# Performance work log

Measured on AMD Instinct MI355X. Metric: run time of the kernel, lower is better.

The kernel has to match this reference:

```python
import jax, jax.numpy as jnp
import numpy as np

N = 100000   # nodes
E = 640000   # edges
D = 128      # in_channels
C = 40       # out_channels (classes)


def setup_inputs() -> dict:
    key = jax.random.key(0)
    ks = jax.random.split(key, 6)
    x = jax.random.normal(ks[0], (N, D), jnp.float32)
    edge_index = jax.random.randint(ks[1], (2, E), 0, N)
    edge_weight = jax.random.uniform(ks[2], (E,), jnp.float32)
    # 8 block convs (4 blocks x 2) stacked, + final conv
    Wb = jax.random.normal(ks[3], (8, D, D), jnp.float32) / np.sqrt(D)
    bb = jnp.zeros((8, D), jnp.float32)
    Wf = jax.random.normal(ks[4], (D, C), jnp.float32) / np.sqrt(D)
    bf = jnp.zeros((C,), jnp.float32)
    return dict(x=x, edge_index=edge_index, edge_weight=edge_weight,
                Wb=Wb, bb=bb, Wf=Wf, bf=bf)


def _gcn(x, W, b, src, dst, w):
    """PyG GCNConv (normalize=True) with self-loops already appended to src/dst/w."""
    n = x.shape[0]
    h = x @ W                                   # [N, out]
    deg = jax.ops.segment_sum(w, dst, num_segments=n)
    dinv = jnp.where(deg > 0, jax.lax.rsqrt(deg), 0.0)
    norm = dinv[src] * w * dinv[dst]            # [E+N]
    out = jax.ops.segment_sum(h[src] * norm[:, None], dst, num_segments=n)
    return out + b


def reference(x, edge_index, edge_weight, Wb, bb, Wf, bf):
    n = x.shape[0]
    loop = jnp.arange(n)
    src = jnp.concatenate([edge_index[0], loop])
    dst = jnp.concatenate([edge_index[1], loop])
    w = jnp.concatenate([edge_weight, jnp.ones((n,), x.dtype)])
    # forward only runs blocks 1-4 (blocks 5-7 unused in the original forward)
    for i in range(4):
        identity = x
        x = jax.nn.relu(_gcn(x, Wb[2 * i], bb[2 * i], src, dst, w))
        # dropout: identity in eval mode
        x = jax.nn.relu(_gcn(x, Wb[2 * i + 1], bb[2 * i + 1], src, dst, w))
        # F.normalize: row-wise L2 with eps=1e-12
        x = x / jnp.maximum(jnp.linalg.norm(x, axis=1, keepdims=True), 1e-12)
        x = (x + identity) / 2
    x = _gcn(x, Wf, bf, src, dst, w)
    return jax.nn.log_softmax(x, axis=1)
```

## Files before the change

### kernel.cpp

```cpp
#include <hip/hip_runtime.h>
#include <math.h>

#define NN 100000
#define EE 640000
#define DD 128
#define CC 40
#define FIXS 4194304.0f

typedef __bf16 bf16x8 __attribute__((ext_vector_type(8)));
typedef float f32x4 __attribute__((ext_vector_type(4)));
typedef unsigned short us8 __attribute__((ext_vector_type(8)));

__device__ inline unsigned short f2b(float f) {
    union { float f; unsigned u; } v; v.f = f;
    unsigned u = v.u;
    return (unsigned short)((u + 0x7FFFu + ((u >> 16) & 1u)) >> 16);
}
__device__ inline float b2f(unsigned short b) {
    union { unsigned u; float f; } v; v.u = ((unsigned)b) << 16;
    return v.f;
}


__global__ __launch_bounds__(256) void k_edge1(const int* __restrict__ dst,
                                               const float* __restrict__ w,
                                               unsigned long long* __restrict__ degcnt,
                                               int* __restrict__ pos) {
    int e = blockIdx.x * 256 + threadIdx.x;
    if (e < EE) {
        int d = dst[e];
        unsigned long long pk =
            ((unsigned long long)(unsigned)(w[e] * FIXS) << 32) | 1ull;
        unsigned long long old = atomicAdd(&degcnt[d], pk);
        pos[e] = (int)(old & 0xffffffffull);
    }
}

__global__ __launch_bounds__(256) void k_scan1p(const unsigned long long* __restrict__ degcnt,
                                                float* __restrict__ dinv,
                                                int* __restrict__ out,
                                                int* __restrict__ partial,
                                                const float* __restrict__ Wb,
                                                const float* __restrict__ Wf,
                                                unsigned short* __restrict__ WT,
                                                unsigned short* __restrict__ WfT) {
    int t = threadIdx.x;
    if (blockIdx.x >= 98) {
        int idx = (blockIdx.x - 98) * 256 + t;
        if (idx < 8 * DD * DD) {
            int m = idx >> 14;
            int n = (idx >> 7) & 127;
            int k = idx & 127;
            WT[idx] = f2b(Wb[(size_t)m * DD * DD + (size_t)k * DD + n]);
        } else {
            int j = idx - 8 * DD * DD;
            if (j < 64 * DD) {
                int n = j >> 7;
                int k = j & 127;
                WfT[j] = (n < CC) ? f2b(Wf[(size_t)k * CC + n]) : 0;
            }
        }
        return;
    }
    __shared__ int lds[256];
    int base = blockIdx.x * 1024 + t * 4;
    int v[4]; int s = 0;
    #pragma unroll
    for (int j = 0; j < 4; ++j) {
        int idx = base + j;
        unsigned long long dc = (idx < NN) ? degcnt[idx] : 0ull;
        v[j] = (int)(dc & 0xffffffffull);
        s += v[j];
        if (idx < NN)
            dinv[idx] = rsqrtf((float)(unsigned)(dc >> 32) * (1.0f / FIXS) + 1.0f);
    }
    lds[t] = s;
    __syncthreads();
    for (int off = 1; off < 256; off <<= 1) {
        int x = lds[t];
        int y = (t >= off) ? lds[t - off] : 0;
        __syncthreads();
        lds[t] = x + y;
        __syncthreads();
    }
    int excl = lds[t] - s;
    if (t == 255) partial[blockIdx.x] = lds[255];
    int run = excl;
    #pragma unroll
    for (int j = 0; j < 4; ++j) {
        int idx = base + j;
        if (idx < NN) out[idx] = run;
        run += v[j];
    }
}

__global__ __launch_bounds__(256) void k_scan3(int* __restrict__ rp,
                                               const int* __restrict__ partial) {
    __shared__ int lds[128];
    int t = threadIdx.x;
    if (t < 128) lds[t] = (t < 98) ? partial[t] : 0;
    __syncthreads();
    for (int off = 1; off < 128; off <<= 1) {
        int x = (t < 128) ? lds[t] : 0;
        int y = (t >= off && t < 128) ? lds[t - off] : 0;
        __syncthreads();
        if (t < 128) lds[t] = x + y;
        __syncthreads();
    }
    int i = blockIdx.x * 256 + t;
    if (i < NN) {
        int c = i >> 10;
        int add = c ? lds[c - 1] : 0;
        rp[i] += add;
    }
    if (i == 0) rp[NN] = EE;
}

__global__ __launch_bounds__(256) void k_scatter(const int* __restrict__ src,
                                                 const int* __restrict__ dst,
                                                 const float* __restrict__ w,
                                                 const float* __restrict__ dinv,
                                                 const int* __restrict__ rp,
                                                 const int* __restrict__ pos,
                                                 int2* __restrict__ cvp) {
    int e = blockIdx.x * 256 + threadIdx.x;
    if (e < EE) {
        int s = src[e], d = dst[e];
        int p = rp[d] + pos[e];
        int2 cv;
        cv.x = s;
        cv.y = __float_as_int(dinv[s] * w[e] * dinv[d]);
        cvp[p] = cv;
    }
}


#define MM_EPILOGUE_128(H_)                                                  \
    {                                                                        \
        _Pragma("unroll")                                                    \
        for (int n = 0; n < 8; ++n) {                                        \
            _Pragma("unroll")                                                \
            for (int v = 0; v < 4; ++v)                                      \
                tb[wid][g * 4 + v][n * 16 + sl] = f2b(acc[n][v]);            \
        }                                                                    \
        __syncthreads();                                                     \
        _Pragma("unroll")                                                    \
        for (int c4 = 0; c4 < 4; ++c4) {                                     \
            int chunk = c4 * 64 + lane;                                      \
            int row = chunk >> 4, seg = chunk & 15;                          \
            int grow = r0 + row;                                             \
            if (grow < NN)                                                   \
                *(us8*)(H_ + (size_t)grow * DD + seg * 8) =                  \
                    *(const us8*)(&tb[wid][row][seg * 8]);                   \
        }                                                                    \
    }

__global__ __launch_bounds__(256) void k_mmx(const float* __restrict__ x,
                                             const unsigned short* __restrict__ WT,
                                             unsigned short* __restrict__ Abf,
                                             unsigned short* __restrict__ H) {
    __shared__ unsigned short tb[4][16][136];
    int wid = threadIdx.x >> 6;
    int lane = threadIdx.x & 63;
    int r0 = blockIdx.x * 64 + wid * 16;
    int sl = lane & 15, g = lane >> 4;
    int arow = r0 + sl;
    bool avalid = arow < NN;
    if (!avalid) arow = NN - 1;

    f32x4 acc[8];
    #pragma unroll
    for (int n = 0; n < 8; ++n) acc[n] = (f32x4){0.f, 0.f, 0.f, 0.f};

    const float* xrow = x + (size_t)arow * DD;
    #pragma unroll
    for (int kc = 0; kc < 4; ++kc) {
        int chunk = kc * 4 + g;
        float4 lo = *(const float4*)(xrow + chunk * 8);
        float4 hi = *(const float4*)(xrow + chunk * 8 + 4);
        us8 r;
        r[0] = f2b(lo.x); r[1] = f2b(lo.y); r[2] = f2b(lo.z); r[3] = f2b(lo.w);
        r[4] = f2b(hi.x); r[5] = f2b(hi.y); r[6] = f2b(hi.z); r[7] = f2b(hi.w);
        if (avalid) ((us8*)(Abf + (size_t)arow * DD))[chunk] = r;
        bf16x8 a = *(bf16x8*)&r;
        #pragma unroll
        for (int n = 0; n < 8; ++n) {
            const bf16x8* wrow = (const bf16x8*)(WT + (size_t)(n * 16 + sl) * DD);
            bf16x8 b = wrow[kc * 4 + g];
            acc[n] = __builtin_amdgcn_mfma_f32_16x16x32_bf16(a, b, acc[n], 0, 0, 0);
        }
    }
    MM_EPILOGUE_128(H);
}

__global__ __launch_bounds__(256) void k_mm_mfma(const unsigned short* __restrict__ X,
                                                 const unsigned short* __restrict__ WT,
                                                 unsigned short* __restrict__ H) {
    __shared__ unsigned short tb[4][16][136];
    int wid = threadIdx.x >> 6;
    int lane = threadIdx.x & 63;
    int r0 = blockIdx.x * 64 + wid * 16;
    int sl = lane & 15, g = lane >> 4;
    int arow = r0 + sl;
    if (arow >= NN) arow = NN - 1;

    f32x4 acc[8];
    #pragma unroll
    for (int n = 0; n < 8; ++n) acc[n] = (f32x4){0.f, 0.f, 0.f, 0.f};

    const bf16x8* xrow = (const bf16x8*)(X + (size_t)arow * DD);
    #pragma unroll
    for (int kc = 0; kc < 4; ++kc) {
        bf16x8 a = xrow[kc * 4 + g];
        #pragma unroll
        for (int n = 0; n < 8; ++n) {
            const bf16x8* wrow = (const bf16x8*)(WT + (size_t)(n * 16 + sl) * DD);
            bf16x8 b = wrow[kc * 4 + g];
            acc[n] = __builtin_amdgcn_mfma_f32_16x16x32_bf16(a, b, acc[n], 0, 0, 0);
        }
    }
    MM_EPILOGUE_128(H);
}

__global__ __launch_bounds__(256) void k_mm40b(const unsigned short* __restrict__ X,
                                               const unsigned short* __restrict__ WfT,
                                               unsigned short* __restrict__ H) {
    int wid = threadIdx.x >> 6;
    int lane = threadIdx.x & 63;
    int r0 = blockIdx.x * 64 + wid * 16;
    int sl = lane & 15, g = lane >> 4;
    int arow = r0 + sl;
    if (arow >= NN) arow = NN - 1;

    f32x4 acc[4];
    #pragma unroll
    for (int n = 0; n < 4; ++n) acc[n] = (f32x4){0.f, 0.f, 0.f, 0.f};

    const bf16x8* xrow = (const bf16x8*)(X + (size_t)arow * DD);
    #pragma unroll
    for (int kc = 0; kc < 4; ++kc) {
        bf16x8 a = xrow[kc * 4 + g];
        #pragma unroll
        for (int n = 0; n < 4; ++n) {
            const bf16x8* wrow = (const bf16x8*)(WfT + (size_t)(n * 16 + sl) * DD);
            bf16x8 b = wrow[kc * 4 + g];
            acc[n] = __builtin_amdgcn_mfma_f32_16x16x32_bf16(a, b, acc[n], 0, 0, 0);
        }
    }
    #pragma unroll
    for (int n = 0; n < 4; ++n) {
        #pragma unroll
        for (int v = 0; v < 4; ++v) {
            int row = r0 + g * 4 + v;
            if (row < NN) H[(size_t)row * 64 + n * 16 + sl] = f2b(acc[n][v]);
        }
    }
}


#define AGG_CORE(h_, node_, sl_, a_, STRIDE_)                               \
    {                                                                       \
        float dv = dinv[node_];                                             \
        float dv2 = dv * dv;                                                \
        us8 m_ = ((const us8*)(h_ + (size_t)node_ * STRIDE_))[sl_];         \
        _Pragma("unroll")                                                   \
        for (int j = 0; j < 8; ++j) a_[j] = dv2 * b2f(m_[j]);               \
        int e = rp[node_], end = rp[node_ + 1];                             \
        for (; e + 4 <= end; e += 4) {                                      \
            int2 c0 = cvp[e], c1 = cvp[e + 1], c2 = cvp[e + 2], c3 = cvp[e + 3]; \
            us8 q0 = ((const us8*)(h_ + (size_t)c0.x * STRIDE_))[sl_];      \
            us8 q1 = ((const us8*)(h_ + (size_t)c1.x * STRIDE_))[sl_];      \
            us8 q2 = ((const us8*)(h_ + (size_t)c2.x * STRIDE_))[sl_];      \
            us8 q3 = ((const us8*)(h_ + (size_t)c3.x * STRIDE_))[sl_];      \
            float v0 = __int_as_float(c0.y), v1 = __int_as_float(c1.y);     \
            float v2 = __int_as_float(c2.y), v3 = __int_as_float(c3.y);     \
            _Pragma("unroll")                                               \
            for (int j = 0; j < 8; ++j)                                     \
                a_[j] += (v0 * b2f(q0[j]) + v1 * b2f(q1[j]))                \
                       + (v2 * b2f(q2[j]) + v3 * b2f(q3[j]));               \
        }                                                                   \
        for (; e < end; ++e) {                                              \
            int2 c0 = cvp[e];                                               \
            us8 q0 = ((const us8*)(h_ + (size_t)c0.x * STRIDE_))[sl_];      \
            float v0 = __int_as_float(c0.y);                                \
            _Pragma("unroll")                                               \
            for (int j = 0; j < 8; ++j) a_[j] += v0 * b2f(q0[j]);           \
        }                                                                   \
    }

__global__ __launch_bounds__(256) void k_agg128(const unsigned short* __restrict__ h,
                                                const float* __restrict__ dinv,
                                                const int* __restrict__ rp,
                                                const int2* __restrict__ cvp,
                                                const float* __restrict__ bias,
                                                unsigned short* __restrict__ outb) {
    int node = blockIdx.x * 16 + (threadIdx.x >> 4);
    int sl = threadIdx.x & 15;
    if (node >= NN) return;
    float a[8];
    AGG_CORE(h, node, sl, a, DD);
    float4 bz0 = ((const float4*)bias)[sl * 2];
    float4 bz1 = ((const float4*)bias)[sl * 2 + 1];
    float bb[8] = {bz0.x, bz0.y, bz0.z, bz0.w, bz1.x, bz1.y, bz1.z, bz1.w};
    us8 r;
    #pragma unroll
    for (int j = 0; j < 8; ++j) r[j] = f2b(fmaxf(a[j] + bb[j], 0.f));
    ((us8*)(outb + (size_t)node * DD))[sl] = r;
}

__global__ __launch_bounds__(256) void k_agg128_nr(const unsigned short* __restrict__ h,
                                                   const float* __restrict__ dinv,
                                                   const int* __restrict__ rp,
                                                   const int2* __restrict__ cvp,
                                                   const float* __restrict__ bias,
                                                   unsigned short* __restrict__ Abf) {
    int node = blockIdx.x * 16 + (threadIdx.x >> 4);
    int sl = threadIdx.x & 15;
    if (node >= NN) return;
    float a[8];
    AGG_CORE(h, node, sl, a, DD);
    float4 bz0 = ((const float4*)bias)[sl * 2];
    float4 bz1 = ((const float4*)bias)[sl * 2 + 1];
    float bb[8] = {bz0.x, bz0.y, bz0.z, bz0.w, bz1.x, bz1.y, bz1.z, bz1.w};
    float ss = 0.f;
    #pragma unroll
    for (int j = 0; j < 8; ++j) {
        a[j] = fmaxf(a[j] + bb[j], 0.f);
        ss += a[j] * a[j];
    }
    ss += __shfl_xor(ss, 1);
    ss += __shfl_xor(ss, 2);
    ss += __shfl_xor(ss, 4);
    ss += __shfl_xor(ss, 8);
    float sc = 1.0f / fmaxf(sqrtf(ss), 1e-12f);
    us8 oldb = ((const us8*)(Abf + (size_t)node * DD))[sl];
    us8 rb;
    #pragma unroll
    for (int j = 0; j < 8; ++j)
        rb[j] = f2b((a[j] * sc + b2f(oldb[j])) * 0.5f);
    ((us8*)(Abf + (size_t)node * DD))[sl] = rb;
}

__global__ __launch_bounds__(256) void k_agg_final(const unsigned short* __restrict__ h,
                                                   const float* __restrict__ dinv,
                                                   const int* __restrict__ rp,
                                                   const int2* __restrict__ cvp,
                                                   const float* __restrict__ bias,
                                                   float* __restrict__ out) {
    int node = blockIdx.x * 32 + (threadIdx.x >> 3);
    int sl = threadIdx.x & 7;
    if (node >= NN) return;
    float a[8];
    AGG_CORE(h, node, sl, a, 64);
    bool real = sl < 5;
    float vv[8];
    if (real) {
        float4 bz0 = ((const float4*)bias)[sl * 2];
        float4 bz1 = ((const float4*)bias)[sl * 2 + 1];
        float bb[8] = {bz0.x, bz0.y, bz0.z, bz0.w, bz1.x, bz1.y, bz1.z, bz1.w};
        #pragma unroll
        for (int j = 0; j < 8; ++j) vv[j] = a[j] + bb[j];
    } else {
        #pragma unroll
        for (int j = 0; j < 8; ++j) vv[j] = -3.0e38f;
    }
    float m = vv[0];
    #pragma unroll
    for (int j = 1; j < 8; ++j) m = fmaxf(m, vv[j]);
    m = fmaxf(m, __shfl_xor(m, 1));
    m = fmaxf(m, __shfl_xor(m, 2));
    m = fmaxf(m, __shfl_xor(m, 4));
    float s = 0.f;
    if (real) {
        #pragma unroll
        for (int j = 0; j < 8; ++j) s += expf(vv[j] - m);
    }
    s += __shfl_xor(s, 1);
    s += __shfl_xor(s, 2);
    s += __shfl_xor(s, 4);
    float ls = m + logf(s);
    if (real) {
        float4 o0 = {vv[0] - ls, vv[1] - ls, vv[2] - ls, vv[3] - ls};
        float4 o1 = {vv[4] - ls, vv[5] - ls, vv[6] - ls, vv[7] - ls};
        float* orow = out + (size_t)node * CC + sl * 8;
        *(float4*)(orow) = o0;
        *(float4*)(orow + 4) = o1;
    }
}


extern "C" void kernel_launch(void* const* d_in, const int* in_sizes, int n_in,
                              void* d_out, int out_size, void* d_ws, size_t ws_size,
                              hipStream_t stream) {
    const float* x  = (const float*)d_in[0];
    const int*   ei = (const int*)d_in[1];
    const float* ew = (const float*)d_in[2];
    const float* Wb = (const float*)d_in[3];
    const float* bb = (const float*)d_in[4];
    const float* Wf = (const float*)d_in[5];
    const float* bf_ = (const float*)d_in[6];
    const int* src = ei;
    const int* dst = ei + EE;
    float* out = (float*)d_out;

    char* p = (char*)d_ws;
    unsigned short*     Abf    = (unsigned short*)p;     p += (size_t)NN * DD * 2;
    unsigned short*     Bbf    = (unsigned short*)p;     p += (size_t)NN * DD * 2;
    unsigned short*     Cbf    = (unsigned short*)p;     p += (size_t)NN * DD * 2;
    unsigned short*     H48    = (unsigned short*)p;     p += (size_t)NN * 64 * 2;
    unsigned short*     WT     = (unsigned short*)p;     p += (size_t)8 * DD * DD * 2;
    unsigned short*     WfT    = (unsigned short*)p;     p += (size_t)64 * DD * 2;
    unsigned long long* degcnt = (unsigned long long*)p; p += (size_t)NN * 8;
    float* dinv = (float*)p; p += (size_t)NN * 4;
    int*   rp   = (int*)p;   p += (size_t)(NN + 1) * 4;
    int*   pos  = (int*)p;   p += (size_t)EE * 4;
    int2*  cvp  = (int2*)p;  p += (size_t)EE * 8;
    int*   partial = (int*)p; p += 128 * 4;

    hipMemsetAsync(degcnt, 0, (size_t)NN * 8, stream);

    k_edge1<<<(EE + 255) / 256, 256, 0, stream>>>(dst, ew, degcnt, pos);
    k_scan1p<<<98 + (8 * DD * DD + 64 * DD + 255) / 256, 256, 0, stream>>>(
        degcnt, dinv, rp, partial, Wb, Wf, WT, WfT);
    k_scan3<<<(NN + 255) / 256, 256, 0, stream>>>(rp, partial);
    k_scatter<<<(EE + 255) / 256, 256, 0, stream>>>(src, dst, ew, dinv, rp, pos, cvp);

    int gb = (NN + 63) / 64;
    k_mmx<<<gb, 256, 0, stream>>>(x, WT, Abf, Bbf);
    for (int blk = 0; blk < 4; ++blk) {
        k_agg128<<<(NN + 15) / 16, 256, 0, stream>>>(Bbf, dinv, rp, cvp,
                                                     bb + (size_t)(2 * blk) * DD, Cbf);
        k_mm_mfma<<<gb, 256, 0, stream>>>(Cbf, WT + (size_t)(2 * blk + 1) * DD * DD, Bbf);
        k_agg128_nr<<<(NN + 15) / 16, 256, 0, stream>>>(Bbf, dinv, rp, cvp,
                                                        bb + (size_t)(2 * blk + 1) * DD, Abf);
        if (blk < 3)
            k_mm_mfma<<<gb, 256, 0, stream>>>(Abf, WT + (size_t)(2 * blk + 2) * DD * DD, Bbf);
    }
    k_mm40b<<<gb, 256, 0, stream>>>(Abf, WfT, H48);
    k_agg_final<<<(NN + 31) / 32, 256, 0, stream>>>(H48, dinv, rp, cvp, bf_, out);
}
```

Measured before the change: 637.0 us.

## Split x conversion into standalone kernel, drop epilogue barrier, stage final matmul stores

Replaces the fused fp32-to-bf16 conversion plus first matmul with a separate elementwise conversion kernel followed by the generic bf16 MFMA matmul. Removes the __syncthreads from the matmul epilogue, since each wave reads only its own shared-memory slice. Also stages the 40-class matmul output through shared memory so it can be written with 16-byte row stores instead of scattered 2-byte writes. The split adds one launch and an extra read of the bf16 copy of x, and dropping the barrier relies on the compiler honoring intra-wave LDS ordering.

Measured after the change: 646.3 us. About the same (+1.5%).

```diff
diff --git a/kernel.cpp b/kernel.cpp
--- a/kernel.cpp
+++ b/kernel.cpp
@@ -134,6 +134,16 @@
     }
 }
 
+__global__ __launch_bounds__(256) void k_x2bf(const float* __restrict__ x,
+                                              unsigned short* __restrict__ Abf) {
+    int idx = blockIdx.x * 256 + threadIdx.x;
+    if (idx >= NN * DD / 4) return;
+    float4 v = ((const float4*)x)[idx];
+    ushort4 r;
+    r.x = f2b(v.x); r.y = f2b(v.y); r.z = f2b(v.z); r.w = f2b(v.w);
+    ((ushort4*)Abf)[idx] = r;
+}
+
 
 #define MM_EPILOGUE_128(H_)                                                  \
     {                                                                        \
@@ -143,7 +153,6 @@
             for (int v = 0; v < 4; ++v)                                      \
                 tb[wid][g * 4 + v][n * 16 + sl] = f2b(acc[n][v]);            \
         }                                                                    \
-        __syncthreads();                                                     \
         _Pragma("unroll")                                                    \
         for (int c4 = 0; c4 < 4; ++c4) {                                     \
             int chunk = c4 * 64 + lane;                                      \
@@ -154,44 +163,6 @@
                     *(const us8*)(&tb[wid][row][seg * 8]);                   \
         }                                                                    \
     }
-
-__global__ __launch_bounds__(256) void k_mmx(const float* __restrict__ x,
-                                             const unsigned short* __restrict__ WT,
-                                             unsigned short* __restrict__ Abf,
-                                             unsigned short* __restrict__ H) {
-    __shared__ unsigned short tb[4][16][136];
-    int wid = threadIdx.x >> 6;
-    int lane = threadIdx.x & 63;
-    int r0 = blockIdx.x * 64 + wid * 16;
-    int sl = lane & 15, g = lane >> 4;
-    int arow = r0 + sl;
-    bool avalid = arow < NN;
-    if (!avalid) arow = NN - 1;
-
-    f32x4 acc[8];
-    #pragma unroll
-    for (int n = 0; n < 8; ++n) acc[n] = (f32x4){0.f, 0.f, 0.f, 0.f};
-
-    const float* xrow = x + (size_t)arow * DD;
-    #pragma unroll
-    for (int kc = 0; kc < 4; ++kc) {
-        int chunk = kc * 4 + g;
-        float4 lo = *(const float4*)(xrow + chunk * 8);
-        float4 hi = *(const float4*)(xrow + chunk * 8 + 4);
-        us8 r;
-        r[0] = f2b(lo.x); r[1] = f2b(lo.y); r[2] = f2b(lo.z); r[3] = f2b(lo.w);
-        r[4] = f2b(hi.x); r[5] = f2b(hi.y); r[6] = f2b(hi.z); r[7] = f2b(hi.w);
-        if (avalid) ((us8*)(Abf + (size_t)arow * DD))[chunk] = r;
-        bf16x8 a = *(bf16x8*)&r;
-        #pragma unroll
-        for (int n = 0; n < 8; ++n) {
-            const bf16x8* wrow = (const bf16x8*)(WT + (size_t)(n * 16 + sl) * DD);
-            bf16x8 b = wrow[kc * 4 + g];
-            acc[n] = __builtin_amdgcn_mfma_f32_16x16x32_bf16(a, b, acc[n], 0, 0, 0);
-        }
-    }
-    MM_EPILOGUE_128(H);
-}
 
 __global__ __launch_bounds__(256) void k_mm_mfma(const unsigned short* __restrict__ X,
                                                  const unsigned short* __restrict__ WT,
@@ -225,6 +196,7 @@
 __global__ __launch_bounds__(256) void k_mm40b(const unsigned short* __restrict__ X,
                                                const unsigned short* __restrict__ WfT,
                                                unsigned short* __restrict__ H) {
+    __shared__ unsigned short tb[4][16][72];
     int wid = threadIdx.x >> 6;
     int lane = threadIdx.x & 63;
     int r0 = blockIdx.x * 64 + wid * 16;
@@ -250,10 +222,17 @@
     #pragma unroll
     for (int n = 0; n < 4; ++n) {
         #pragma unroll
-        for (int v = 0; v < 4; ++v) {
-            int row = r0 + g * 4 + v;
-            if (row < NN) H[(size_t)row * 64 + n * 16 + sl] = f2b(acc[n][v]);
-        }
+        for (int v = 0; v < 4; ++v)
+            tb[wid][g * 4 + v][n * 16 + sl] = f2b(acc[n][v]);
+    }
+    #pragma unroll
+    for (int c4 = 0; c4 < 2; ++c4) {
+        int chunk = c4 * 64 + lane;
+        int row = chunk >> 3, seg = chunk & 7;
+        int grow = r0 + row;
+        if (grow < NN)
+            *(us8*)(H + (size_t)grow * 64 + seg * 8) =
+                *(const us8*)(&tb[wid][row][seg * 8]);
     }
 }
 
@@ -424,9 +403,10 @@
         degcnt, dinv, rp, partial, Wb, Wf, WT, WfT);
     k_scan3<<<(NN + 255) / 256, 256, 0, stream>>>(rp, partial);
     k_scatter<<<(EE + 255) / 256, 256, 0, stream>>>(src, dst, ew, dinv, rp, pos, cvp);
+    k_x2bf<<<(NN * DD / 4 + 255) / 256, 256, 0, stream>>>(x, Abf);
 
     int gb = (NN + 63) / 64;
-    k_mmx<<<gb, 256, 0, stream>>>(x, WT, Abf, Bbf);
+    k_mm_mfma<<<gb, 256, 0, stream>>>(Abf, WT, Bbf);
     for (int blk = 0; blk < 4; ++blk) {
         k_agg128<<<(NN + 15) / 16, 256, 0, stream>>>(Bbf, dinv, rp, cvp,
                                                      bb + (size_t)(2 * blk) * DD, Cbf);
```
